# Kernel optimization log

Measured on AMD Instinct MI355X. Metric: run time of the kernel, lower is better.

## Reference

```python
import jax, jax.numpy as jnp
import numpy as np

BATCH, SEQ, DIM = 8, 2048, 512
NUM_Q, CODEBOOK = 8, 1024


def setup_inputs() -> dict:
    key = jax.random.key(0)
    k1, k2 = jax.random.split(key)
    x = jax.random.normal(k1, (BATCH, SEQ, DIM), dtype=jnp.float32)
    # one codebook per quantizer (uniform codebook size -> stacked [q, c, d])
    codebooks = jax.random.normal(k2, (NUM_Q, CODEBOOK, DIM), dtype=jnp.float32)
    return {"x": x, "codebooks": codebooks}


def reference(x, codebooks):
    """Residual VQ (Algorithm 1, SoundStream). Sequential nearest-neighbor
    quantization of the residual with straight-through estimator.
    project_in/project_out are Identity (codebook_dim == dim).
    Returns (quantized_out [b,n,d], indices [b,n,q], commit_losses [q]).
    """
    residual = x
    quantized_out = jnp.zeros_like(x)
    all_indices = []
    all_losses = []
    num_q = codebooks.shape[0]
    for q in range(num_q):  # small fixed loop over quantizer layers
        cb = codebooks[q]  # [c, d]
        # argmin of squared euclidean distance; ||r||^2 is constant over codes
        scores = -2.0 * jnp.einsum('bnd,cd->bnc', residual, cb) \
                 + jnp.sum(cb * cb, axis=-1)  # [b, n, c]
        idx = jnp.argmin(scores, axis=-1)  # [b, n]
        quant = cb[idx]  # gather codes: [b, n, d]
        # commitment loss (mse of detached quantize vs layer input)
        commit = jnp.mean((jax.lax.stop_gradient(quant) - residual) ** 2)
        # straight-through estimator
        quant_st = residual + jax.lax.stop_gradient(quant - residual)
        quantized_out = quantized_out + quant_st
        residual = residual - jax.lax.stop_gradient(quant)
        all_indices.append(idx)
        all_losses.append(commit)
    indices = jnp.stack(all_indices, axis=-1)  # [b, n, q]
    losses = jnp.stack(all_losses)  # [q]
    return quantized_out, indices, losses
```

## Files before the change

### kernel.cpp

```cpp
#include <hip/hip_runtime.h>
#include <cstdint>
#include <cstddef>


#define BATCH 8
#define SEQ   2048
#define DIM   512
#define NUMQ  8
#define CODES 1024
#define NPTS  (BATCH*SEQ)
#define MPTS  64
#define NWG   (NPTS/MPTS)
#define NTHR  512
#define NCHUNK 32
#define CHUNK_BYTES 32768

#define OUT_IDX   (BATCH*SEQ*DIM)
#define OUT_LOSS  (OUT_IDX + BATCH*SEQ*NUMQ)

#define WS_LOSS   0
#define WS_CNORM  1024
#define WS_CBH    40960
#define WS_CNORMD (WS_CBH + NUMQ*NCHUNK*CHUNK_BYTES)

typedef _Float16 f16x8  __attribute__((ext_vector_type(8)));
typedef _Float16 f16x4  __attribute__((ext_vector_type(4)));
typedef float    f32x16 __attribute__((ext_vector_type(16)));

__global__ void k_prep(const float* __restrict__ cb, unsigned char* __restrict__ cbH,
                       float* __restrict__ cnorm, double* __restrict__ cnd,
                       double* __restrict__ loss) {
  unsigned u = blockIdx.x * blockDim.x + threadIdx.x;
  {
    unsigned h  = u & 1;
    unsigned v  = u >> 1;
    unsigned c  = v & 127;
    unsigned g  = (v >> 7) & 1;
    unsigned w  = (v >> 8) & 7;
    unsigned ks = (v >> 11) & 31;
    unsigned q  = v >> 16;
    unsigned code = (w << 7) | c;
    unsigned k = ks * 16 + g * 8 + h * 4;
    float4 val = *(const float4*)(cb + ((size_t)((q << 10) | code)) * DIM + k);
    f16x4 o;
    o[0] = (_Float16)val.x; o[1] = (_Float16)val.y;
    o[2] = (_Float16)val.z; o[3] = (_Float16)val.w;
    *(f16x4*)(cbH + (size_t)u * 8) = o;
  }
  if (u < NUMQ) loss[u] = 0.0;
  if (u < NUMQ * CODES) {
    const float4* row = (const float4*)(cb + (size_t)u * DIM);
    float s = 0.f;
    double d0 = 0, d1 = 0, d2 = 0, d3 = 0;
    for (int i = 0; i < 128; i += 4) {
      float4 a = row[i], b = row[i + 1], c2 = row[i + 2], d = row[i + 3];
      s += a.x * a.x + a.y * a.y + a.z * a.z + a.w * a.w
         + b.x * b.x + b.y * b.y + b.z * b.z + b.w * b.w
         + c2.x * c2.x + c2.y * c2.y + c2.z * c2.z + c2.w * c2.w
         + d.x * d.x + d.y * d.y + d.z * d.z + d.w * d.w;
      d0 += (double)a.x * a.x + (double)a.y * a.y + (double)a.z * a.z + (double)a.w * a.w;
      d1 += (double)b.x * b.x + (double)b.y * b.y + (double)b.z * b.z + (double)b.w * b.w;
      d2 += (double)c2.x * c2.x + (double)c2.y * c2.y + (double)c2.z * c2.z + (double)c2.w * c2.w;
      d3 += (double)d.x * d.x + (double)d.y * d.y + (double)d.z * d.z + (double)d.w * d.w;
    }
    cnorm[u] = s;
    cnd[u] = (d0 + d1) + (d2 + d3);
  }
}

struct BF { f16x8 b0, b1, b2, b3; };
__device__ __forceinline__ BF loadB(const unsigned char* __restrict__ p) {
  BF r;
  r.b0 = *(const f16x8*)(p);
  r.b1 = *(const f16x8*)(p + 512);
  r.b2 = *(const f16x8*)(p + 1024);
  r.b3 = *(const f16x8*)(p + 1536);
  return r;
}

__launch_bounds__(NTHR, 2)
__global__ void k_main(const float* __restrict__ x, const float* __restrict__ cb,
                       const unsigned char* __restrict__ cbH,
                       const float* __restrict__ cnorm,
                       const double* __restrict__ cnormd,
                       double* __restrict__ lossAcc,
                       float* __restrict__ out)
{
  __shared__ __align__(16) unsigned char Af[MPTS * DIM * 2];
  __shared__ float          s1w[MPTS][8];
  __shared__ unsigned short id1w[MPTS][8];
  __shared__ unsigned short cand[MPTS][8][4];
  __shared__ unsigned char  ccnt[MPTS][8];
  __shared__ float          gmA[MPTS];
  __shared__ int            win0A[MPTS];
  __shared__ unsigned short idxs[MPTS][NUMQ];
  __shared__ double         lred[8];

  const int tid = threadIdx.x;
  const int cl  = tid & 63;
  const int w   = tid >> 6;
  const int l31 = cl & 31;
  const int l5  = cl >> 5;
  const int wg  = blockIdx.x;

  const int rp = tid >> 3;
  const int rj = tid & 7;
  const size_t gp = (size_t)wg * MPTS + rp;
  float4 r4[16];
  {
    const float4* xr = (const float4*)(x + gp * DIM + rj * 64);
    #pragma unroll
    for (int i = 0; i < 16; ++i) r4[i] = xr[i];
  }

  for (int q = 0; q < NUMQ; ++q) {
    const unsigned char* bq = cbH + ((size_t)q << 20) + (w << 12) + (l5 << 11) + (l31 << 4);

    BF s0 = loadB(bq);
    BF s1 = loadB(bq + CHUNK_BYTES);

    #pragma unroll
    for (int i = 0; i < 8; ++i) {
      float4 a = r4[2 * i], b = r4[2 * i + 1];
      f16x8 v;
      v[0] = (_Float16)a.x; v[1] = (_Float16)a.y; v[2] = (_Float16)a.z; v[3] = (_Float16)a.w;
      v[4] = (_Float16)b.x; v[5] = (_Float16)b.y; v[6] = (_Float16)b.z; v[7] = (_Float16)b.w;
      int sl = ((i << 3) | rj) ^ (rp & 31);
      *(f16x8*)(Af + rp * 1024 + (sl << 4)) = v;
    }
    __syncthreads();

    f32x16 acc[2][4];
    #pragma unroll
    for (int mt = 0; mt < 2; ++mt)
      #pragma unroll
      for (int nt = 0; nt < 4; ++nt)
        #pragma unroll
        for (int e = 0; e < 16; ++e) acc[mt][nt][e] = 0.0f;

    #pragma unroll 1
    for (int kk = 0; kk < 16; ++kk) {
      const int ks = kk << 1;
      {
        const int s5 = (ks << 1) | l5;
        const int sf = ((((s5 & 7) << 3) | (s5 >> 3)) ^ l31) << 4;
        f16x8 a0 = *(const f16x8*)(Af + l31 * 1024 + sf);
        f16x8 a1 = *(const f16x8*)(Af + 32768 + l31 * 1024 + sf);
        __builtin_amdgcn_s_setprio(1);
        acc[0][0] = __builtin_amdgcn_mfma_f32_32x32x16_f16(a0, s0.b0, acc[0][0], 0, 0, 0);
        acc[0][1] = __builtin_amdgcn_mfma_f32_32x32x16_f16(a0, s0.b1, acc[0][1], 0, 0, 0);
        acc[0][2] = __builtin_amdgcn_mfma_f32_32x32x16_f16(a0, s0.b2, acc[0][2], 0, 0, 0);
        acc[0][3] = __builtin_amdgcn_mfma_f32_32x32x16_f16(a0, s0.b3, acc[0][3], 0, 0, 0);
        acc[1][0] = __builtin_amdgcn_mfma_f32_32x32x16_f16(a1, s0.b0, acc[1][0], 0, 0, 0);
        acc[1][1] = __builtin_amdgcn_mfma_f32_32x32x16_f16(a1, s0.b1, acc[1][1], 0, 0, 0);
        acc[1][2] = __builtin_amdgcn_mfma_f32_32x32x16_f16(a1, s0.b2, acc[1][2], 0, 0, 0);
        acc[1][3] = __builtin_amdgcn_mfma_f32_32x32x16_f16(a1, s0.b3, acc[1][3], 0, 0, 0);
        __builtin_amdgcn_s_setprio(0);
        if (ks + 2 < NCHUNK) s0 = loadB(bq + (size_t)(ks + 2) * CHUNK_BYTES);
      }
      {
        const int ks1 = ks + 1;
        const int s5 = (ks1 << 1) | l5;
        const int sf = ((((s5 & 7) << 3) | (s5 >> 3)) ^ l31) << 4;
        f16x8 a0 = *(const f16x8*)(Af + l31 * 1024 + sf);
        f16x8 a1 = *(const f16x8*)(Af + 32768 + l31 * 1024 + sf);
        __builtin_amdgcn_s_setprio(1);
        acc[0][0] = __builtin_amdgcn_mfma_f32_32x32x16_f16(a0, s1.b0, acc[0][0], 0, 0, 0);
        acc[0][1] = __builtin_amdgcn_mfma_f32_32x32x16_f16(a0, s1.b1, acc[0][1], 0, 0, 0);
        acc[0][2] = __builtin_amdgcn_mfma_f32_32x32x16_f16(a0, s1.b2, acc[0][2], 0, 0, 0);
        acc[0][3] = __builtin_amdgcn_mfma_f32_32x32x16_f16(a0, s1.b3, acc[0][3], 0, 0, 0);
        acc[1][0] = __builtin_amdgcn_mfma_f32_32x32x16_f16(a1, s1.b0, acc[1][0], 0, 0, 0);
        acc[1][1] = __builtin_amdgcn_mfma_f32_32x32x16_f16(a1, s1.b1, acc[1][1], 0, 0, 0);
        acc[1][2] = __builtin_amdgcn_mfma_f32_32x32x16_f16(a1, s1.b2, acc[1][2], 0, 0, 0);
        acc[1][3] = __builtin_amdgcn_mfma_f32_32x32x16_f16(a1, s1.b3, acc[1][3], 0, 0, 0);
        __builtin_amdgcn_s_setprio(0);
        if (ks1 + 2 < NCHUNK) s1 = loadB(bq + (size_t)(ks1 + 2) * CHUNK_BYTES);
      }
    }

    {
      const float* cnq = cnorm + (q << 10) + (w << 7) + l31;
      const float cn0 = cnq[0], cn1 = cnq[32], cn2 = cnq[64], cn3 = cnq[96];
      #pragma unroll
      for (int mt = 0; mt < 2; ++mt) {
        acc[mt][0] = acc[mt][0] * -2.0f + cn0;
        acc[mt][1] = acc[mt][1] * -2.0f + cn1;
        acc[mt][2] = acc[mt][2] * -2.0f + cn2;
        acc[mt][3] = acc[mt][3] * -2.0f + cn3;
      }
    }

    #pragma unroll
    for (int mt = 0; mt < 2; ++mt)
      #pragma unroll
      for (int r = 0; r < 16; ++r) {
        float s = acc[mt][0][r]; int bi = l31;
        if (acc[mt][1][r] < s) { s = acc[mt][1][r]; bi = 32 + l31; }
        if (acc[mt][2][r] < s) { s = acc[mt][2][r]; bi = 64 + l31; }
        if (acc[mt][3][r] < s) { s = acc[mt][3][r]; bi = 96 + l31; }
        float smin = s;
        #pragma unroll
        for (int m = 1; m < 32; m <<= 1) smin = fminf(smin, __shfl_xor(smin, m));
        unsigned long long bm = __ballot(s == smin);
        unsigned half = l5 ? (unsigned)(bm >> 32) : (unsigned)bm;
        int first = __builtin_ctz(half) + (l5 << 5);
        int id = __shfl(bi, first);
        if (l31 == 0) {
          int p = mt * 32 + (r & 3) + 8 * (r >> 2) + 4 * l5;
          s1w[p][w] = smin; id1w[p][w] = (unsigned short)id;
        }
      }
    __syncthreads();

    if (tid < MPTS) {
      int p = tid;
      float bs = s1w[p][0]; int bi = id1w[p][0];
      #pragma unroll
      for (int ww = 1; ww < 8; ++ww) {
        float s = s1w[p][ww];
        if (s < bs) { bs = s; bi = ww * 128 + id1w[p][ww]; }
      }
      gmA[p] = bs; win0A[p] = bi;
    }
    __syncthreads();

    #pragma unroll
    for (int mt = 0; mt < 2; ++mt)
      #pragma unroll
      for (int r = 0; r < 16; ++r) {
        const int p0 = mt * 32 + (r & 3) + 8 * (r >> 2);
        const float g0 = gmA[p0], g1 = gmA[p0 + 4];
        const float lim0 = g0 + 1.5f + 1e-4f * fabsf(g0);
        const float lim1 = g1 + 1.5f + 1e-4f * fabsf(g1);
        const float lim = l5 ? lim1 : lim0;
        unsigned long long b0 = __ballot(acc[mt][0][r] <= lim);
        unsigned long long b1 = __ballot(acc[mt][1][r] <= lim);
        unsigned long long b2 = __ballot(acc[mt][2][r] <= lim);
        unsigned long long b3 = __ballot(acc[mt][3][r] <= lim);
        if (cl == 0 || cl == 32) {
          const int p = p0 + (cl >> 3);
          unsigned short* cd = &cand[p][w][0];
          unsigned m0 = (cl == 0) ? (unsigned)b0 : (unsigned)(b0 >> 32);
          unsigned m1 = (cl == 0) ? (unsigned)b1 : (unsigned)(b1 >> 32);
          unsigned m2 = (cl == 0) ? (unsigned)b2 : (unsigned)(b2 >> 32);
          unsigned m3 = (cl == 0) ? (unsigned)b3 : (unsigned)(b3 >> 32);
          int n = 0;
          while (m0 && n < 4) { int bt = __builtin_ctz(m0); m0 &= m0 - 1; cd[n++] = (unsigned short)(bt); }
          while (m1 && n < 4) { int bt = __builtin_ctz(m1); m1 &= m1 - 1; cd[n++] = (unsigned short)(32 + bt); }
          while (m2 && n < 4) { int bt = __builtin_ctz(m2); m2 &= m2 - 1; cd[n++] = (unsigned short)(64 + bt); }
          while (m3 && n < 4) { int bt = __builtin_ctz(m3); m3 &= m3 - 1; cd[n++] = (unsigned short)(96 + bt); }
          ccnt[p][w] = (unsigned char)n;
        }
      }
    __syncthreads();

    {
      const int g  = cl >> 3;
      const int gl = cl & 7;
      const int p  = (w << 3) + g;
      int tot = 0;
      #pragma unroll
      for (int ww = 0; ww < 8; ++ww) tot += ccnt[p][ww];
      int winner = win0A[p];
      int mtot = tot;
      #pragma unroll
      for (int m = 1; m < 64; m <<= 1) { int o = __shfl_xor(mtot, m); if (o > mtot) mtot = o; }
      if (mtot > 1) {
        double bs = 1.0e300, bs2 = 1.0e300; int bi = 0x7FFFFFFF;
        #pragma unroll 1
        for (int k = 0; k < mtot; ++k) {
          int cc = -1;
          if (tot > 1 && k < tot) {
            int rem = k, ww = 0;
            #pragma unroll 1
            for (; ww < 7; ++ww) { int nn = ccnt[p][ww]; if (rem < nn) break; rem -= nn; }
            cc = ww * 128 + cand[p][ww][rem];
          }
          double dt = 0.0;
          if (cc >= 0) {
            const float4* cr = (const float4*)(cb + ((size_t)q * CODES + cc) * DIM + gl * 64);
            double d0 = 0, d1 = 0, d2 = 0, d3 = 0;
            #pragma unroll
            for (int i = 0; i < 16; i += 4) {
              float4 c0 = cr[i], c1 = cr[i + 1], c2 = cr[i + 2], c3 = cr[i + 3];
              d0 += (double)r4[i].x * c0.x + (double)r4[i].y * c0.y
                  + (double)r4[i].z * c0.z + (double)r4[i].w * c0.w;
              d1 += (double)r4[i + 1].x * c1.x + (double)r4[i + 1].y * c1.y
                  + (double)r4[i + 1].z * c1.z + (double)r4[i + 1].w * c1.w;
              d2 += (double)r4[i + 2].x * c2.x + (double)r4[i + 2].y * c2.y
                  + (double)r4[i + 2].z * c2.z + (double)r4[i + 2].w * c2.w;
              d3 += (double)r4[i + 3].x * c3.x + (double)r4[i + 3].y * c3.y
                  + (double)r4[i + 3].z * c3.z + (double)r4[i + 3].w * c3.w;
            }
            dt = (d0 + d1) + (d2 + d3);
          }
          #pragma unroll
          for (int m = 1; m < 8; m <<= 1) dt += __shfl_xor(dt, m);
          if (cc >= 0) {
            double s = -2.0 * dt + cnormd[(q << 10) + cc];
            if (s < bs) { bs2 = bs; bs = s; bi = cc; }
            else if (s < bs2) { bs2 = s; }
          }
        }
        if (tot > 1 && bs2 - bs <= 1e-3 + 1e-6 * fabs(bs)) {
          bs = 1.0e300; bi = 0x7FFFFFFF;
          const float4* xr2 = (const float4*)(x + gp * DIM + gl * 64);
          #pragma unroll 1
          for (int k = 0; k < tot; ++k) {
            int rem = k, ww = 0;
            #pragma unroll 1
            for (; ww < 7; ++ww) { int nn = ccnt[p][ww]; if (rem < nn) break; rem -= nn; }
            const int cc = ww * 128 + cand[p][ww][rem];
            const float4* cr = (const float4*)(cb + ((size_t)q * CODES + cc) * DIM + gl * 64);
            double dt = 0.0;
            #pragma unroll 1
            for (int i = 0; i < 16; ++i) {
              float4 xv = xr2[i];
              double rhx = xv.x, rhy = xv.y, rhz = xv.z, rhw = xv.w;
              #pragma unroll 1
              for (int t2 = 0; t2 < q; ++t2) {
                const float4* qr = (const float4*)(cb + ((size_t)t2 * CODES + idxs[p][t2]) * DIM + gl * 64);
                float4 qv = qr[i];
                rhx -= (double)qv.x; rhy -= (double)qv.y;
                rhz -= (double)qv.z; rhw -= (double)qv.w;
              }
              float4 cv = cr[i];
              dt += rhx * cv.x + rhy * cv.y + rhz * cv.z + rhw * cv.w;
            }
            #pragma unroll
            for (int m = 1; m < 8; m <<= 1) dt += __shfl_xor(dt, m);
            double s = -2.0 * dt + cnormd[(q << 10) + cc];
            if (s < bs || (s == bs && cc < bi)) { bs = s; bi = cc; }
          }
        }
        if (tot > 1) winner = bi;
      }
      if (gl == 0) idxs[p][q] = (unsigned short)winner;
    }
    __syncthreads();

    {
      const int win = idxs[rp][q];
      const float4* cr = (const float4*)(cb + ((size_t)q * CODES + win) * DIM + rj * 64);
      double ls0 = 0.0, ls1 = 0.0;
      #pragma unroll
      for (int i = 0; i < 16; i += 2) {
        float4 c0 = cr[i], c1 = cr[i + 1];
        float dx0 = c0.x - r4[i].x, dy0 = c0.y - r4[i].y;
        float dz0 = c0.z - r4[i].z, dw0 = c0.w - r4[i].w;
        ls0 += (double)dx0 * dx0 + (double)dy0 * dy0 + (double)dz0 * dz0 + (double)dw0 * dw0;
        r4[i].x -= c0.x; r4[i].y -= c0.y; r4[i].z -= c0.z; r4[i].w -= c0.w;
        float dx1 = c1.x - r4[i + 1].x, dy1 = c1.y - r4[i + 1].y;
        float dz1 = c1.z - r4[i + 1].z, dw1 = c1.w - r4[i + 1].w;
        ls1 += (double)dx1 * dx1 + (double)dy1 * dy1 + (double)dz1 * dz1 + (double)dw1 * dw1;
        r4[i + 1].x -= c1.x; r4[i + 1].y -= c1.y; r4[i + 1].z -= c1.z; r4[i + 1].w -= c1.w;
      }
      double ls = ls0 + ls1;
      #pragma unroll
      for (int m = 1; m < 64; m <<= 1) ls += __shfl_xor(ls, m);
      if (cl == 0) lred[w] = ls;
      __syncthreads();
      if (tid == 0) {
        double t = lred[0] + lred[1] + lred[2] + lred[3]
                 + lred[4] + lred[5] + lred[6] + lred[7];
        atomicAdd(lossAcc + q, t);
      }
      __syncthreads();
    }
  }

  {
    const float4* xr = (const float4*)(x + gp * DIM + rj * 64);
    float4* orow = (float4*)(out + gp * DIM + rj * 64);
    #pragma unroll
    for (int i = 0; i < 16; ++i) {
      float4 xv = xr[i];
      float4 o;
      o.x = xv.x - r4[i].x; o.y = xv.y - r4[i].y;
      o.z = xv.z - r4[i].z; o.w = xv.w - r4[i].w;
      orow[i] = o;
    }
  }
  if (tid < MPTS) {
    float* ob = out + OUT_IDX + ((size_t)wg * MPTS + tid) * NUMQ;
    #pragma unroll
    for (int j = 0; j < NUMQ; ++j) ob[j] = (float)idxs[tid][j];
  }
}

__global__ void k_fin(const double* __restrict__ loss, float* __restrict__ out) {
  int t = threadIdx.x;
  if (t < NUMQ)
    out[OUT_LOSS + t] = (float)(loss[t] / (double)((size_t)BATCH * SEQ * DIM));
}

extern "C" void kernel_launch(void* const* d_in, const int* in_sizes, int n_in,
                              void* d_out, int out_size, void* d_ws, size_t ws_size,
                              hipStream_t stream) {
  (void)in_sizes; (void)n_in; (void)out_size; (void)ws_size;
  const float* x  = (const float*)d_in[0];
  const float* cb = (const float*)d_in[1];
  float* out = (float*)d_out;
  char* ws = (char*)d_ws;
  double* loss = (double*)(ws + WS_LOSS);
  float* cnorm = (float*)(ws + WS_CNORM);
  unsigned char* cbH = (unsigned char*)(ws + WS_CBH);
  double* cnormd = (double*)(ws + WS_CNORMD);

  k_prep<<<NUMQ * NCHUNK * CHUNK_BYTES / 8 / 256, 256, 0, stream>>>(
      cb, cbH, cnorm, cnormd, loss);
  k_main<<<NWG, NTHR, 0, stream>>>(x, cb, cbH, cnorm, cnormd, loss, out);
  k_fin<<<1, 64, 0, stream>>>(loss, out);
}
```

Measured before the change: 524.0 us.

## Fuse prep, main and finalize kernels into one cooperative launch with grid syncs

Merges the codebook fp16 conversion and norm precompute, the main quantization kernel, and the loss finalization into a single cooperative kernel. Phases are separated by grid-wide barriers. The aim is to remove two extra kernel launches and their gaps. In exchange it needs all 256 workgroups of 512 threads resident at once, and the grid syncs add their own cost. The prep work now runs inside a kernel whose launch bounds target high register use.

```diff
diff --git a/kernel.cpp b/kernel.cpp
--- a/kernel.cpp
+++ b/kernel.cpp
@@ -1,7 +1,10 @@
 #include <hip/hip_runtime.h>
+#include <hip/hip_cooperative_groups.h>
 #include <cstdint>
 #include <cstddef>
 
+
+namespace cg = cooperative_groups;
 
 #define BATCH 8
 #define SEQ   2048
@@ -27,47 +30,6 @@
 typedef _Float16 f16x4  __attribute__((ext_vector_type(4)));
 typedef float    f32x16 __attribute__((ext_vector_type(16)));
 
-__global__ void k_prep(const float* __restrict__ cb, unsigned char* __restrict__ cbH,
-                       float* __restrict__ cnorm, double* __restrict__ cnd,
-                       double* __restrict__ loss) {
-  unsigned u = blockIdx.x * blockDim.x + threadIdx.x;
-  {
-    unsigned h  = u & 1;
-    unsigned v  = u >> 1;
-    unsigned c  = v & 127;
-    unsigned g  = (v >> 7) & 1;
-    unsigned w  = (v >> 8) & 7;
-    unsigned ks = (v >> 11) & 31;
-    unsigned q  = v >> 16;
-    unsigned code = (w << 7) | c;
-    unsigned k = ks * 16 + g * 8 + h * 4;
-    float4 val = *(const float4*)(cb + ((size_t)((q << 10) | code)) * DIM + k);
-    f16x4 o;
-    o[0] = (_Float16)val.x; o[1] = (_Float16)val.y;
-    o[2] = (_Float16)val.z; o[3] = (_Float16)val.w;
-    *(f16x4*)(cbH + (size_t)u * 8) = o;
-  }
-  if (u < NUMQ) loss[u] = 0.0;
-  if (u < NUMQ * CODES) {
-    const float4* row = (const float4*)(cb + (size_t)u * DIM);
-    float s = 0.f;
-    double d0 = 0, d1 = 0, d2 = 0, d3 = 0;
-    for (int i = 0; i < 128; i += 4) {
-      float4 a = row[i], b = row[i + 1], c2 = row[i + 2], d = row[i + 3];
-      s += a.x * a.x + a.y * a.y + a.z * a.z + a.w * a.w
-         + b.x * b.x + b.y * b.y + b.z * b.z + b.w * b.w
-         + c2.x * c2.x + c2.y * c2.y + c2.z * c2.z + c2.w * c2.w
-         + d.x * d.x + d.y * d.y + d.z * d.z + d.w * d.w;
-      d0 += (double)a.x * a.x + (double)a.y * a.y + (double)a.z * a.z + (double)a.w * a.w;
-      d1 += (double)b.x * b.x + (double)b.y * b.y + (double)b.z * b.z + (double)b.w * b.w;
-      d2 += (double)c2.x * c2.x + (double)c2.y * c2.y + (double)c2.z * c2.z + (double)c2.w * c2.w;
-      d3 += (double)d.x * d.x + (double)d.y * d.y + (double)d.z * d.z + (double)d.w * d.w;
-    }
-    cnorm[u] = s;
-    cnd[u] = (d0 + d1) + (d2 + d3);
-  }
-}
-
 struct BF { f16x8 b0, b1, b2, b3; };
 __device__ __forceinline__ BF loadB(const unsigned char* __restrict__ p) {
   BF r;
@@ -79,12 +41,12 @@
 }
 
 __launch_bounds__(NTHR, 2)
-__global__ void k_main(const float* __restrict__ x, const float* __restrict__ cb,
-                       const unsigned char* __restrict__ cbH,
-                       const float* __restrict__ cnorm,
-                       const double* __restrict__ cnormd,
-                       double* __restrict__ lossAcc,
-                       float* __restrict__ out)
+__global__ void k_fused(const float* __restrict__ x, const float* __restrict__ cb,
+                        unsigned char* __restrict__ cbH,
+                        float* __restrict__ cnorm,
+                        double* __restrict__ cnormd,
+                        double* __restrict__ lossAcc,
+                        float* __restrict__ out)
 {
   __shared__ __align__(16) unsigned char Af[MPTS * DIM * 2];
   __shared__ float          s1w[MPTS][8];
@@ -97,11 +59,54 @@
   __shared__ double         lred[8];
 
   const int tid = threadIdx.x;
+  const int wg  = blockIdx.x;
+
+  {
+    const unsigned tg = wg * NTHR + tid;
+    #pragma unroll
+    for (int j = 0; j < 8; ++j) {
+      unsigned u = tg * 8 + j;
+      unsigned h  = u & 1;
+      unsigned v  = u >> 1;
+      unsigned c  = v & 127;
+      unsigned g  = (v >> 7) & 1;
+      unsigned w2 = (v >> 8) & 7;
+      unsigned ks = (v >> 11) & 31;
+      unsigned q2 = v >> 16;
+      unsigned code = (w2 << 7) | c;
+      unsigned k = ks * 16 + g * 8 + h * 4;
+      float4 val = *(const float4*)(cb + ((size_t)((q2 << 10) | code)) * DIM + k);
+      f16x4 o;
+      o[0] = (_Float16)val.x; o[1] = (_Float16)val.y;
+      o[2] = (_Float16)val.z; o[3] = (_Float16)val.w;
+      *(f16x4*)(cbH + (size_t)u * 8) = o;
+    }
+    if (tg < NUMQ) lossAcc[tg] = 0.0;
+    if (tg < NUMQ * CODES) {
+      const float4* row = (const float4*)(cb + (size_t)tg * DIM);
+      float s = 0.f;
+      double d0 = 0, d1 = 0, d2 = 0, d3 = 0;
+      for (int i = 0; i < 128; i += 4) {
+        float4 a = row[i], b = row[i + 1], c2 = row[i + 2], d = row[i + 3];
+        s += a.x * a.x + a.y * a.y + a.z * a.z + a.w * a.w
+           + b.x * b.x + b.y * b.y + b.z * b.z + b.w * b.w
+           + c2.x * c2.x + c2.y * c2.y + c2.z * c2.z + c2.w * c2.w
+           + d.x * d.x + d.y * d.y + d.z * d.z + d.w * d.w;
+        d0 += (double)a.x * a.x + (double)a.y * a.y + (double)a.z * a.z + (double)a.w * a.w;
+        d1 += (double)b.x * b.x + (double)b.y * b.y + (double)b.z * b.z + (double)b.w * b.w;
+        d2 += (double)c2.x * c2.x + (double)c2.y * c2.y + (double)c2.z * c2.z + (double)c2.w * c2.w;
+        d3 += (double)d.x * d.x + (double)d.y * d.y + (double)d.z * d.z + (double)d.w * d.w;
+      }
+      cnorm[tg] = s;
+      cnormd[tg] = (d0 + d1) + (d2 + d3);
+    }
+  }
+  cg::this_grid().sync();
+
   const int cl  = tid & 63;
   const int w   = tid >> 6;
   const int l31 = cl & 31;
   const int l5  = cl >> 5;
-  const int wg  = blockIdx.x;
 
   const int rp = tid >> 3;
   const int rj = tid & 7;
@@ -386,12 +391,12 @@
     #pragma unroll
     for (int j = 0; j < NUMQ; ++j) ob[j] = (float)idxs[tid][j];
   }
-}
-
-__global__ void k_fin(const double* __restrict__ loss, float* __restrict__ out) {
-  int t = threadIdx.x;
-  if (t < NUMQ)
-    out[OUT_LOSS + t] = (float)(loss[t] / (double)((size_t)BATCH * SEQ * DIM));
+
+  cg::this_grid().sync();
+  if (wg == 0 && tid < NUMQ) {
+    double v = atomicAdd(lossAcc + tid, 0.0);
+    out[OUT_LOSS + tid] = (float)(v / (double)((size_t)BATCH * SEQ * DIM));
+  }
 }
 
 extern "C" void kernel_launch(void* const* d_in, const int* in_sizes, int n_in,
@@ -407,8 +412,8 @@
   unsigned char* cbH = (unsigned char*)(ws + WS_CBH);
   double* cnormd = (double*)(ws + WS_CNORMD);
 
-  k_prep<<<NUMQ * NCHUNK * CHUNK_BYTES / 8 / 256, 256, 0, stream>>>(
-      cb, cbH, cnorm, cnormd, loss);
-  k_main<<<NWG, NTHR, 0, stream>>>(x, cb, cbH, cnorm, cnormd, loss, out);
-  k_fin<<<1, 64, 0, stream>>>(loss, out);
+  void* args[] = { (void*)&x, (void*)&cb, (void*)&cbH, (void*)&cnorm,
+                   (void*)&cnormd, (void*)&loss, (void*)&out };
+  hipLaunchCooperativeKernel((const void*)k_fused, dim3(NWG), dim3(NTHR),
+                             args, 0, stream);
 }
```

Result: slower. 602.6 us (+15.0%).
